# Kernel tuning notes

Measured on AMD Instinct MI355X. Metric: run time of the kernel, lower is better.

Reference implementation:

```python
import jax, jax.numpy as jnp
import numpy as np

D_MODEL = 1024
NUM_HEADS = 16
HEAD_DIM = D_MODEL // NUM_HEADS
THETA = 10000.0


def _rope(x):
    # x: [B, H, S, Dk]; interleaved even/odd rotation as in the torch module
    *_, seq_len, d_k = x.shape
    d = d_k // 2
    inv_freq = 1.0 / (THETA ** (2.0 * jnp.arange(d, dtype=jnp.float32) / d_k))
    pos = jnp.arange(seq_len, dtype=jnp.float32)
    angles = pos[:, None] * inv_freq[None, :]  # [S, d]
    cos = jnp.cos(angles)
    sin = jnp.sin(angles)
    x_even = x[..., 0::2]
    x_odd = x[..., 1::2]
    rot_even = x_even * cos - x_odd * sin
    rot_odd = x_even * sin + x_odd * cos
    return jnp.stack([rot_even, rot_odd], axis=-1).reshape(x.shape)


def setup_inputs() -> dict:
    key = jax.random.key(0)
    ks = jax.random.split(key, 5)
    B, S = 4, 2048
    x = jax.random.normal(ks[0], (B, S, D_MODEL), dtype=jnp.float32)
    q_w = jax.random.uniform(ks[1], (D_MODEL, D_MODEL), dtype=jnp.float32)
    k_w = jax.random.uniform(ks[2], (D_MODEL, D_MODEL), dtype=jnp.float32)
    v_w = jax.random.uniform(ks[3], (D_MODEL, D_MODEL), dtype=jnp.float32)
    o_w = jax.random.uniform(ks[4], (D_MODEL, D_MODEL), dtype=jnp.float32)
    return {"x": x, "q_w": q_w, "k_w": k_w, "v_w": v_w, "o_w": o_w}


def reference(x, q_w, k_w, v_w, o_w):
    B, S, _ = x.shape
    def split_heads(t):
        return t.reshape(B, S, NUM_HEADS, HEAD_DIM).transpose(0, 2, 1, 3)  # [B,H,S,Dk]
    Q = split_heads(x @ q_w.T)
    K = split_heads(x @ k_w.T)
    V = split_heads(x @ v_w.T)
    Q = _rope(Q)
    K = _rope(K)
    scale = 1.0 / jnp.sqrt(jnp.float32(HEAD_DIM))
    scores = jnp.einsum('bhqd,bhkd->bhqk', Q, K) * scale  # [B,H,S,S]
    causal = jnp.tril(jnp.ones((S, S), dtype=bool))
    scores = jnp.where(causal[None, None], scores, -jnp.inf)
    attn = jax.nn.softmax(scores, axis=-1)
    out = jnp.einsum('bhqk,bhkd->bhqd', attn, V)  # [B,H,S,Dk]
    out = out.transpose(0, 2, 1, 3).reshape(B, S, D_MODEL)
    return out @ o_w.T
```

## Files before the change

kernel.cpp:

```cpp
#include <hip/hip_runtime.h>
#include <hip/hip_bf16.h>
#include <cstdint>
#include <cstddef>

#define D_MODEL   1024
#define NUM_HEADS 16
#define HEAD_DIM  64
#define SEQ       2048
#define BATCH     4
#define BH        (BATCH*NUM_HEADS)
#define MROWS     (BATCH*SEQ)

typedef _Float16 half8  __attribute__((ext_vector_type(8)));
typedef _Float16 half4v __attribute__((ext_vector_type(4)));
typedef float    floatx4 __attribute__((ext_vector_type(4)));

__device__ inline void gld_lds16(const void* g, void* l) {
    __builtin_amdgcn_global_load_lds(
        (__attribute__((address_space(1))) void*)g,
        (__attribute__((address_space(3))) void*)l,
        16, 0, 0);
}

__global__ void rope_table(float2* __restrict__ tab) {
    const int i = blockIdx.x * blockDim.x + threadIdx.x;
    const int p = i & 31, s = i >> 5;
    const double inv = pow(10000.0, -(double)p / 32.0);
    const double ang = (double)s * inv;
    tab[i] = make_float2((float)cos(ang), (float)sin(ang));
}

__global__ void f32_split_f16(const float* __restrict__ in,
                              _Float16* __restrict__ hi,
                              _Float16* __restrict__ lo, int n4) {
    int i = blockIdx.x * blockDim.x + threadIdx.x;
    if (i >= n4) return;
    float4 v = ((const float4*)in)[i];
    half4v h = { (_Float16)v.x, (_Float16)v.y, (_Float16)v.z, (_Float16)v.w };
    half4v l = { (_Float16)(v.x - (float)h.x), (_Float16)(v.y - (float)h.y),
                 (_Float16)(v.z - (float)h.z), (_Float16)(v.w - (float)h.w) };
    ((half4v*)hi)[i] = h;
    ((half4v*)lo)[i] = l;
}

__global__ void conv_weights(const float* __restrict__ qw, const float* __restrict__ kw,
                             const float* __restrict__ vw, const float* __restrict__ ow,
                             _Float16* __restrict__ qwh, _Float16* __restrict__ qwl,
                             _Float16* __restrict__ kwh, _Float16* __restrict__ kwl,
                             _Float16* __restrict__ vwh, _Float16* __restrict__ owh) {
    const int i = blockIdx.x * blockDim.x + threadIdx.x;
    const int which = i >> 18;
    const int j = i & 262143;
    const float4 v = ((const float4*)(which == 0 ? qw : which == 1 ? kw :
                                      which == 2 ? vw : ow))[j];
    half4v h = { (_Float16)v.x, (_Float16)v.y, (_Float16)v.z, (_Float16)v.w };
    if (which < 2) {
        half4v l = { (_Float16)(v.x - (float)h.x), (_Float16)(v.y - (float)h.y),
                     (_Float16)(v.z - (float)h.z), (_Float16)(v.w - (float)h.w) };
        ((half4v*)(which ? kwh : qwh))[j] = h;
        ((half4v*)(which ? kwl : qwl))[j] = l;
    } else {
        ((half4v*)(which == 2 ? vwh : owh))[j] = h;
    }
}

__global__ __launch_bounds__(256)
void gemm_bt(const _Float16* __restrict__ A, const _Float16* __restrict__ B,
             float* __restrict__ Cout, int M, int N, int K) {
    __shared__ _Float16 As[128*32];
    __shared__ _Float16 Bs[128*32];

    const int nb = N >> 7;
    const int bx = blockIdx.x % nb;
    const int by = blockIdx.x / nb;
    const int m0 = by << 7, n0 = bx << 7;

    const int t    = threadIdx.x;
    const int w    = t >> 6;
    const int lane = t & 63;
    const int r    = lane & 15;
    const int quad = lane >> 4;
    const int wm   = (w >> 1) << 6;
    const int wn   = (w & 1) << 6;

    const int srow = lane >> 2;
    const int scol = (lane & 3) << 3;

    floatx4 acc[4][4];
    #pragma unroll
    for (int i = 0; i < 4; i++)
        #pragma unroll
        for (int j = 0; j < 4; j++)
            acc[i][j] = (floatx4){0.f, 0.f, 0.f, 0.f};

    for (int k0 = 0; k0 < K; k0 += 32) {
        __syncthreads();
        #pragma unroll
        for (int p = 0; p < 2; ++p) {
            const int rbase = p*64 + w*16;
            gld_lds16(&A[(size_t)(m0 + rbase + srow)*K + k0 + scol], &As[rbase*32]);
            gld_lds16(&B[(size_t)(n0 + rbase + srow)*K + k0 + scol], &Bs[rbase*32]);
        }
        __syncthreads();

        half8 af[4], bf[4];
        #pragma unroll
        for (int i = 0; i < 4; i++)
            af[i] = *(const half8*)&As[(wm + i*16 + r)*32 + quad*8];
        #pragma unroll
        for (int j = 0; j < 4; j++)
            bf[j] = *(const half8*)&Bs[(wn + j*16 + r)*32 + quad*8];

        #pragma unroll
        for (int i = 0; i < 4; i++)
            #pragma unroll
            for (int j = 0; j < 4; j++)
                acc[i][j] = __builtin_amdgcn_mfma_f32_16x16x32_f16(
                                af[i], bf[j], acc[i][j], 0, 0, 0);
    }

    #pragma unroll
    for (int i = 0; i < 4; i++)
        #pragma unroll
        for (int j = 0; j < 4; j++)
            #pragma unroll
            for (int v = 0; v < 4; v++) {
                const int m = m0 + wm + i*16 + quad*4 + v;
                const int n = n0 + wn + j*16 + r;
                Cout[(size_t)m*N + n] = acc[i][j][v];
            }
}

__global__ __launch_bounds__(256)
void gemm_qkv(const _Float16* __restrict__ Axh, const _Float16* __restrict__ Axl,
              const _Float16* __restrict__ qwh, const _Float16* __restrict__ qwl,
              const _Float16* __restrict__ kwh, const _Float16* __restrict__ kwl,
              const _Float16* __restrict__ vwh,
              _Float16* __restrict__ Qhi, _Float16* __restrict__ Qlo,
              _Float16* __restrict__ Khi, _Float16* __restrict__ Klo,
              _Float16* __restrict__ Vt,  const float2* __restrict__ tab) {
    __shared__ _Float16 smem[4*4096];
    _Float16* Ash = smem;
    _Float16* Asl = smem + 4096;
    _Float16* Bsh = smem + 8192;
    _Float16* Bsl = smem + 12288;

    const int bxa = blockIdx.x;
    const int bx  = bxa % 24;
    const int by  = bxa / 24;
    const int wt  = bx >> 3;
    const int n0  = (bx & 7) << 7;
    const int m0  = by << 7;

    const _Float16* Bh = (wt == 0) ? qwh : (wt == 1) ? kwh : vwh;
    const _Float16* Bl = (wt == 0) ? qwl : kwl;

    const int t    = threadIdx.x;
    const int w    = t >> 6;
    const int lane = t & 63;
    const int r    = lane & 15;
    const int quad = lane >> 4;
    const int wm   = (w >> 1) << 6;
    const int wn   = (w & 1) << 6;

    const int srow = lane >> 2;
    const int scol = (lane & 3) << 3;

    floatx4 acc[4][4];
    #pragma unroll
    for (int i = 0; i < 4; i++)
        #pragma unroll
        for (int j = 0; j < 4; j++)
            acc[i][j] = (floatx4){0.f, 0.f, 0.f, 0.f};

    for (int k0 = 0; k0 < 1024; k0 += 32) {
        __syncthreads();
        #pragma unroll
        for (int p = 0; p < 2; ++p) {
            const int rbase = p*64 + w*16;
            const size_t ga = (size_t)(m0 + rbase + srow)*1024 + k0 + scol;
            const size_t gb = (size_t)(n0 + rbase + srow)*1024 + k0 + scol;
            gld_lds16(&Axh[ga], &Ash[rbase*32]);
            gld_lds16(&Bh [gb], &Bsh[rbase*32]);
            if (wt < 2) {
                gld_lds16(&Axl[ga], &Asl[rbase*32]);
                gld_lds16(&Bl [gb], &Bsl[rbase*32]);
            }
        }
        __syncthreads();

        half8 ah[4], bh[4];
        #pragma unroll
        for (int i = 0; i < 4; i++)
            ah[i] = *(const half8*)&Ash[(wm + i*16 + r)*32 + quad*8];
        #pragma unroll
        for (int j = 0; j < 4; j++)
            bh[j] = *(const half8*)&Bsh[(wn + j*16 + r)*32 + quad*8];

        if (wt < 2) {
            half8 al[4], bl[4];
            #pragma unroll
            for (int i = 0; i < 4; i++)
                al[i] = *(const half8*)&Asl[(wm + i*16 + r)*32 + quad*8];
            #pragma unroll
            for (int j = 0; j < 4; j++)
                bl[j] = *(const half8*)&Bsl[(wn + j*16 + r)*32 + quad*8];
            #pragma unroll
            for (int i = 0; i < 4; i++)
                #pragma unroll
                for (int j = 0; j < 4; j++) {
                    acc[i][j] = __builtin_amdgcn_mfma_f32_16x16x32_f16(
                                    ah[i], bh[j], acc[i][j], 0, 0, 0);
                    acc[i][j] = __builtin_amdgcn_mfma_f32_16x16x32_f16(
                                    ah[i], bl[j], acc[i][j], 0, 0, 0);
                    acc[i][j] = __builtin_amdgcn_mfma_f32_16x16x32_f16(
                                    al[i], bh[j], acc[i][j], 0, 0, 0);
                }
        } else {
            #pragma unroll
            for (int i = 0; i < 4; i++)
                #pragma unroll
                for (int j = 0; j < 4; j++)
                    acc[i][j] = __builtin_amdgcn_mfma_f32_16x16x32_f16(
                                    ah[i], bh[j], acc[i][j], 0, 0, 0);
        }
    }

    __syncthreads();
    float* sc = (float*)smem + w*1088;
    const int g  = lane & 7;
    const int rw = lane >> 3;
    const int hh = (n0 + wn) >> 6;

    if (wt < 2) {
        _Float16* Chi = wt ? Khi : Qhi;
        _Float16* Clo = wt ? Klo : Qlo;
        #pragma unroll
        for (int i = 0; i < 4; i++) {
            #pragma unroll
            for (int j = 0; j < 4; j++)
                #pragma unroll
                for (int v = 0; v < 4; v++)
                    sc[(quad*4 + v)*68 + j*16 + r] = acc[i][j][v];
            #pragma unroll
            for (int rg = 0; rg < 2; rg++) {
                const int row = rw + rg*8;
                const int m   = m0 + wm + i*16 + row;
                const int bb  = m >> 11, s_ = m & 2047;
                const float4 va = *(const float4*)&sc[row*68 + g*8];
                const float4 vb = *(const float4*)&sc[row*68 + g*8 + 4];
                const float vv[8] = {va.x, va.y, va.z, va.w,
                                     vb.x, vb.y, vb.z, vb.w};
                half8 hv, lv;
                #pragma unroll
                for (int p2 = 0; p2 < 4; p2++) {
                    const float2 cs = tab[s_*32 + g*4 + p2];
                    const float e0 = vv[2*p2], o0 = vv[2*p2+1];
                    const float re = e0*cs.x - o0*cs.y;
                    const float ro = e0*cs.y + o0*cs.x;
                    const _Float16 rh = (_Float16)re;
                    const _Float16 oh = (_Float16)ro;
                    hv[2*p2]   = rh; lv[2*p2]   = (_Float16)(re - (float)rh);
                    hv[2*p2+1] = oh; lv[2*p2+1] = (_Float16)(ro - (float)oh);
                }
                const size_t idx = ((((size_t)bb*NUM_HEADS + hh)*SEQ + s_) << 6) + g*8;
                *(half8*)&Chi[idx] = hv;
                *(half8*)&Clo[idx] = lv;
            }
        }
    } else {
        const int d = lane;
        #pragma unroll
        for (int i = 0; i < 4; i++) {
            #pragma unroll
            for (int j = 0; j < 4; j++)
                #pragma unroll
                for (int v = 0; v < 4; v++)
                    sc[(quad*4 + v)*68 + j*16 + r] = acc[i][j][v];
            #pragma unroll
            for (int rg = 0; rg < 2; rg++) {
                const int m  = m0 + wm + i*16 + rg*8;
                const int bb = m >> 11, s_ = m & 2047;
                half8 ov;
                #pragma unroll
                for (int rr = 0; rr < 8; rr++)
                    ov[rr] = (_Float16)sc[(rg*8 + rr)*68 + d];
                *(half8*)&Vt[((((size_t)bb*NUM_HEADS + hh)*HEAD_DIM + d) << 11) + s_] = ov;
            }
        }
    }
}

#define PSTR 72
__global__ __launch_bounds__(256)
void flash_attn(const _Float16* __restrict__ Qhi, const _Float16* __restrict__ Qlo,
                const _Float16* __restrict__ Khi, const _Float16* __restrict__ Klo,
                const _Float16* __restrict__ Vt,  _Float16* __restrict__ AO) {
    __shared__ _Float16 Ksh0[64*32];
    __shared__ _Float16 Ksh1[64*32];
    __shared__ _Float16 Ksl0[64*32];
    __shared__ _Float16 Ksl1[64*32];
    __shared__ _Float16 Vs0 [64*32];
    __shared__ _Float16 Vs1 [64*32];
    __shared__ _Float16 Pl  [4][16*PSTR];

    const int t    = threadIdx.x;
    const int w    = t >> 6;
    const int lane = t & 63;
    const int r    = lane & 15;
    const int quad = lane >> 4;

    const int bx = blockIdx.x;
    const int bh = bx & 63;
    const int qb = 31 - (bx >> 6);
    const int q0w = qb*64 + w*16;
    const int b  = bh >> 4, h = bh & 15;

    const _Float16* Qh_ = Qhi + (size_t)bh * SEQ * HEAD_DIM;
    const _Float16* Ql_ = Qlo + (size_t)bh * SEQ * HEAD_DIM;
    const _Float16* Khg = Khi + (size_t)bh * SEQ * HEAD_DIM;
    const _Float16* Klg = Klo + (size_t)bh * SEQ * HEAD_DIM;
    const _Float16* Vtg = Vt  + (size_t)bh * HEAD_DIM * SEQ;

    half8 qh[2], ql[2];
    #pragma unroll
    for (int c = 0; c < 2; ++c) {
        qh[c] = *(const half8*)&Qh_[(size_t)(q0w + r)*64 + c*32 + quad*8];
        ql[c] = *(const half8*)&Ql_[(size_t)(q0w + r)*64 + c*32 + quad*8];
    }

    floatx4 ot[4];
    #pragma unroll
    for (int dt = 0; dt < 4; ++dt) ot[dt] = (floatx4){0.f,0.f,0.f,0.f};
    float mi = -1e30f, li = 0.f;

    const int sr = lane >> 2;
    const int sc = (lane & 3) << 3;

    const int niter = qb + 1;
    for (int kt = 0; kt < niter; ++kt) {
        const int k0 = kt << 6;

        __syncthreads();
        {
            const int rb  = w << 4;
            const int row = rb + sr;
            const size_t kr = (size_t)(k0 + row)*64;
            gld_lds16(&Khg[kr +      sc], &Ksh0[rb*32]);
            gld_lds16(&Khg[kr + 32 + sc], &Ksh1[rb*32]);
            gld_lds16(&Klg[kr +      sc], &Ksl0[rb*32]);
            gld_lds16(&Klg[kr + 32 + sc], &Ksl1[rb*32]);
            const size_t vr = (size_t)row*SEQ + k0;
            gld_lds16(&Vtg[vr +      sc], &Vs0[rb*32]);
            gld_lds16(&Vtg[vr + 32 + sc], &Vs1[rb*32]);
        }
        __syncthreads();

        float s[16];
        #pragma unroll
        for (int sub = 0; sub < 4; ++sub) {
            floatx4 a = (floatx4){0.f,0.f,0.f,0.f};
            const int fr = (sub*16 + r)*32 + quad*8;
            const half8 kh0 = *(const half8*)&Ksh0[fr];
            const half8 kh1 = *(const half8*)&Ksh1[fr];
            const half8 kl0 = *(const half8*)&Ksl0[fr];
            const half8 kl1 = *(const half8*)&Ksl1[fr];
            a = __builtin_amdgcn_mfma_f32_16x16x32_f16(kh0, qh[0], a, 0, 0, 0);
            a = __builtin_amdgcn_mfma_f32_16x16x32_f16(kh1, qh[1], a, 0, 0, 0);
            a = __builtin_amdgcn_mfma_f32_16x16x32_f16(kh0, ql[0], a, 0, 0, 0);
            a = __builtin_amdgcn_mfma_f32_16x16x32_f16(kh1, ql[1], a, 0, 0, 0);
            a = __builtin_amdgcn_mfma_f32_16x16x32_f16(kl0, qh[0], a, 0, 0, 0);
            a = __builtin_amdgcn_mfma_f32_16x16x32_f16(kl1, qh[1], a, 0, 0, 0);
            #pragma unroll
            for (int v = 0; v < 4; ++v) s[sub*4 + v] = a[v] * 0.125f;
        }

        if (kt == niter - 1) {
            #pragma unroll
            for (int sub = 0; sub < 4; ++sub)
                #pragma unroll
                for (int v = 0; v < 4; ++v)
                    if (k0 + sub*16 + quad*4 + v > q0w + r)
                        s[sub*4 + v] = -1e30f;
        }

        float tm = s[0];
        #pragma unroll
        for (int i = 1; i < 16; ++i) tm = fmaxf(tm, s[i]);
        tm = fmaxf(tm, __shfl_xor(tm, 16));
        tm = fmaxf(tm, __shfl_xor(tm, 32));
        const float mn = fmaxf(mi, tm);
        const float alpha = __expf(mi - mn);
        mi = mn;
        float rs = 0.f;
        #pragma unroll
        for (int i = 0; i < 16; ++i) { s[i] = __expf(s[i] - mn); rs += s[i]; }
        rs += __shfl_xor(rs, 16);
        rs += __shfl_xor(rs, 32);
        li = li*alpha + rs;
        #pragma unroll
        for (int dt = 0; dt < 4; ++dt)
            #pragma unroll
            for (int v = 0; v < 4; ++v) ot[dt][v] *= alpha;

        #pragma unroll
        for (int sub = 0; sub < 4; ++sub) {
            half4v pk = { (_Float16)s[sub*4+0], (_Float16)s[sub*4+1],
                          (_Float16)s[sub*4+2], (_Float16)s[sub*4+3] };
            *(half4v*)&Pl[w][r*PSTR + sub*16 + quad*4] = pk;
        }

        #pragma unroll
        for (int c = 0; c < 2; ++c) {
            const half8 pf = *(const half8*)&Pl[w][r*PSTR + c*32 + quad*8];
            const _Float16* Vsc = c ? Vs1 : Vs0;
            #pragma unroll
            for (int dt = 0; dt < 4; ++dt) {
                const half8 vf = *(const half8*)&Vsc[(dt*16 + r)*32 + quad*8];
                ot[dt] = __builtin_amdgcn_mfma_f32_16x16x32_f16(vf, pf, ot[dt], 0, 0, 0);
            }
        }
    }

    const float inv = 1.0f / li;
    const int q = q0w + r;
    #pragma unroll
    for (int dt = 0; dt < 4; ++dt) {
        half4v o = { (_Float16)(ot[dt][0]*inv), (_Float16)(ot[dt][1]*inv),
                     (_Float16)(ot[dt][2]*inv), (_Float16)(ot[dt][3]*inv) };
        *(half4v*)&AO[((size_t)(b*SEQ + q))*D_MODEL + h*HEAD_DIM + dt*16 + quad*4] = o;
    }
}

extern "C" void kernel_launch(void* const* d_in, const int* in_sizes, int n_in,
                              void* d_out, int out_size, void* d_ws, size_t ws_size,
                              hipStream_t stream) {
    const float* x  = (const float*)d_in[0];
    const float* qw = (const float*)d_in[1];
    const float* kw = (const float*)d_in[2];
    const float* vw = (const float*)d_in[3];
    const float* ow = (const float*)d_in[4];
    float* out = (float*)d_out;

    _Float16* xh  = (_Float16*)d_ws;
    _Float16* xl  = xh  + (size_t)MROWS * D_MODEL;
    _Float16* qwh = xl  + (size_t)MROWS * D_MODEL;
    _Float16* qwl = qwh + (size_t)D_MODEL * D_MODEL;
    _Float16* kwh = qwl + (size_t)D_MODEL * D_MODEL;
    _Float16* kwl = kwh + (size_t)D_MODEL * D_MODEL;
    _Float16* vwh = kwl + (size_t)D_MODEL * D_MODEL;
    _Float16* owh = vwh + (size_t)D_MODEL * D_MODEL;
    _Float16* Qhi = owh + (size_t)D_MODEL * D_MODEL;
    _Float16* Qlo = Qhi + (size_t)MROWS * D_MODEL;
    _Float16* Khi = Qlo + (size_t)MROWS * D_MODEL;
    _Float16* Klo = Khi + (size_t)MROWS * D_MODEL;
    _Float16* Vt  = Klo + (size_t)MROWS * D_MODEL;
    _Float16* AO  = Vt  + (size_t)MROWS * D_MODEL;
    float2*   tab = (float2*)(AO + (size_t)MROWS * D_MODEL);

    rope_table<<<(SEQ*32)/256, 256, 0, stream>>>(tab);

    const int nx4 = MROWS * D_MODEL / 4;
    f32_split_f16<<<nx4/256, 256, 0, stream>>>(x, xh, xl, nx4);
    conv_weights<<<(4*262144)/256, 256, 0, stream>>>(qw, kw, vw, ow,
                                                     qwh, qwl, kwh, kwl, vwh, owh);

    gemm_qkv<<<64*24, 256, 0, stream>>>(xh, xl, qwh, qwl, kwh, kwl, vwh,
                                        Qhi, Qlo, Khi, Klo, Vt, tab);

    flash_attn<<<BH * (SEQ/64), 256, 0, stream>>>(Qhi, Qlo, Khi, Klo, Vt, AO);

    gemm_bt<<<(MROWS/128)*(D_MODEL/128), 256, 0, stream>>>(AO, owh, out,
                                                           MROWS, D_MODEL, D_MODEL);
}
```

Measured before the change: 382.0 us.

## Double-buffer K/V tiles in LDS and raise wave priority around MFMA blocks

The flash attention loop now stages the next K-hi/K-lo/V tile into a second LDS buffer with async global-to-LDS loads while the current tile is being consumed. This removes the second barrier per iteration and is meant to hide global load latency behind the QK and PV MFMA work. It also wraps both MFMA sections in s_setprio(1) so waves issuing matrix instructions get scheduling priority. In exchange, the K/V LDS footprint doubles, which can cut the number of blocks resident per CU and lower occupancy.

```diff
diff --git a/kernel.cpp b/kernel.cpp
--- a/kernel.cpp
+++ b/kernel.cpp
@@ -296,13 +296,8 @@
 void flash_attn(const _Float16* __restrict__ Qhi, const _Float16* __restrict__ Qlo,
                 const _Float16* __restrict__ Khi, const _Float16* __restrict__ Klo,
                 const _Float16* __restrict__ Vt,  _Float16* __restrict__ AO) {
-    __shared__ _Float16 Ksh0[64*32];
-    __shared__ _Float16 Ksh1[64*32];
-    __shared__ _Float16 Ksl0[64*32];
-    __shared__ _Float16 Ksl1[64*32];
-    __shared__ _Float16 Vs0 [64*32];
-    __shared__ _Float16 Vs1 [64*32];
-    __shared__ _Float16 Pl  [4][16*PSTR];
+    __shared__ _Float16 SB[2][6][64*32];
+    __shared__ _Float16 Pl[4][16*PSTR];
 
     const int t    = threadIdx.x;
     const int w    = t >> 6;
@@ -336,35 +331,48 @@
 
     const int sr = lane >> 2;
     const int sc = (lane & 3) << 3;
+    const int rb = w << 4;
+
+    auto stage = [&](int buf, int kt) {
+        const int k0  = kt << 6;
+        const int row = rb + sr;
+        const size_t kr = (size_t)(k0 + row)*64;
+        gld_lds16(&Khg[kr +      sc], &SB[buf][0][rb*32]);
+        gld_lds16(&Khg[kr + 32 + sc], &SB[buf][1][rb*32]);
+        gld_lds16(&Klg[kr +      sc], &SB[buf][2][rb*32]);
+        gld_lds16(&Klg[kr + 32 + sc], &SB[buf][3][rb*32]);
+        const size_t vr = (size_t)row*SEQ + k0;
+        gld_lds16(&Vtg[vr +      sc], &SB[buf][4][rb*32]);
+        gld_lds16(&Vtg[vr + 32 + sc], &SB[buf][5][rb*32]);
+    };
 
     const int niter = qb + 1;
+    stage(0, 0);
+    int cur = 0;
+
     for (int kt = 0; kt < niter; ++kt) {
         const int k0 = kt << 6;
 
         __syncthreads();
-        {
-            const int rb  = w << 4;
-            const int row = rb + sr;
-            const size_t kr = (size_t)(k0 + row)*64;
-            gld_lds16(&Khg[kr +      sc], &Ksh0[rb*32]);
-            gld_lds16(&Khg[kr + 32 + sc], &Ksh1[rb*32]);
-            gld_lds16(&Klg[kr +      sc], &Ksl0[rb*32]);
-            gld_lds16(&Klg[kr + 32 + sc], &Ksl1[rb*32]);
-            const size_t vr = (size_t)row*SEQ + k0;
-            gld_lds16(&Vtg[vr +      sc], &Vs0[rb*32]);
-            gld_lds16(&Vtg[vr + 32 + sc], &Vs1[rb*32]);
-        }
-        __syncthreads();
+        if (kt + 1 < niter) stage(cur ^ 1, kt + 1);
+
+        const _Float16* Kh0 = SB[cur][0];
+        const _Float16* Kh1 = SB[cur][1];
+        const _Float16* Kl0 = SB[cur][2];
+        const _Float16* Kl1 = SB[cur][3];
+        const _Float16* Vp0 = SB[cur][4];
+        const _Float16* Vp1 = SB[cur][5];
 
         float s[16];
+        __builtin_amdgcn_s_setprio(1);
         #pragma unroll
         for (int sub = 0; sub < 4; ++sub) {
             floatx4 a = (floatx4){0.f,0.f,0.f,0.f};
             const int fr = (sub*16 + r)*32 + quad*8;
-            const half8 kh0 = *(const half8*)&Ksh0[fr];
-            const half8 kh1 = *(const half8*)&Ksh1[fr];
-            const half8 kl0 = *(const half8*)&Ksl0[fr];
-            const half8 kl1 = *(const half8*)&Ksl1[fr];
+            const half8 kh0 = *(const half8*)&Kh0[fr];
+            const half8 kh1 = *(const half8*)&Kh1[fr];
+            const half8 kl0 = *(const half8*)&Kl0[fr];
+            const half8 kl1 = *(const half8*)&Kl1[fr];
             a = __builtin_amdgcn_mfma_f32_16x16x32_f16(kh0, qh[0], a, 0, 0, 0);
             a = __builtin_amdgcn_mfma_f32_16x16x32_f16(kh1, qh[1], a, 0, 0, 0);
             a = __builtin_amdgcn_mfma_f32_16x16x32_f16(kh0, ql[0], a, 0, 0, 0);
@@ -374,6 +382,7 @@
             #pragma unroll
             for (int v = 0; v < 4; ++v) s[sub*4 + v] = a[v] * 0.125f;
         }
+        __builtin_amdgcn_s_setprio(0);
 
         if (kt == niter - 1) {
             #pragma unroll
@@ -410,16 +419,20 @@
             *(half4v*)&Pl[w][r*PSTR + sub*16 + quad*4] = pk;
         }
 
+        __builtin_amdgcn_s_setprio(1);
         #pragma unroll
         for (int c = 0; c < 2; ++c) {
             const half8 pf = *(const half8*)&Pl[w][r*PSTR + c*32 + quad*8];
-            const _Float16* Vsc = c ? Vs1 : Vs0;
+            const _Float16* Vsc = c ? Vp1 : Vp0;
             #pragma unroll
             for (int dt = 0; dt < 4; ++dt) {
                 const half8 vf = *(const half8*)&Vsc[(dt*16 + r)*32 + quad*8];
                 ot[dt] = __builtin_amdgcn_mfma_f32_16x16x32_f16(vf, pf, ot[dt], 0, 0, 0);
             }
         }
+        __builtin_amdgcn_s_setprio(0);
+
+        cur ^= 1;
     }
 
     const float inv = 1.0f / li;
```

After: 389.3 us. About the same (+1.9%).
